# Kernel optimization log

Measured on AMD Instinct MI355X. Metric: run time of the kernel, lower is better.

The kernel has to match this reference:

```python
import jax, jax.numpy as jnp
import numpy as np

CHANNELS = [64, 128, 256, 512, 512]
RES = [256, 128, 64, 32, 16]
N = 8          # batch
NQ = 128       # n_quad
NCW = 128      # nc_w (output descriptor size)
GRAD_BOOST = 10.0


def _norm(x):
    # Norm module: per-sample, per-row normalization over last dim; torch std is unbiased (ddof=1)
    m = jnp.mean(x, axis=-1, keepdims=True)
    s = jnp.std(x, axis=-1, ddof=1, keepdims=True)
    return (x - m) / (s + 1e-8)


def _quad(x, w):
    # Quad_module: (M^T @ softmax(grad_boost*w, axis=0))**2, summed over spatial dim
    n, c, h, wd = x.shape
    M = x.reshape(n, c, h * wd)                      # (N, C, HW)
    sm = jax.nn.softmax(w * GRAD_BOOST, axis=0)      # (C, NQ)
    proj = jnp.einsum('nch,co->nho', M, sm)          # (N, HW, NQ)
    return jnp.sum(proj ** 2, axis=1)                # (N, NQ)


def setup_inputs() -> dict:
    key = jax.random.key(0)
    ks = jax.random.split(key, 20)
    inp = {}
    for i, (c, r) in enumerate(zip(CHANNELS, RES)):
        inp[f"x{i}"] = jax.random.normal(ks[i], (N, c, r, r), dtype=jnp.float32)
        # torch init: 5/grad_boost * rand(n_in, n_out) = 0.5 * U[0,1)
        inp[f"w1_{i}"] = 0.5 * jax.random.uniform(ks[5 + i], (c, NQ), dtype=jnp.float32)
    d_in = len(CHANNELS) * NQ
    inp["fc1_w"] = jax.random.normal(ks[10], (d_in, 512), dtype=jnp.float32) * 0.04
    inp["fc1_b"] = jnp.zeros((512,), dtype=jnp.float32)
    inp["fc2_w"] = jax.random.normal(ks[11], (512, 512), dtype=jnp.float32) * 0.04
    inp["fc2_b"] = jnp.zeros((512,), dtype=jnp.float32)
    inp["fc3_w"] = jax.random.normal(ks[12], (512, NCW), dtype=jnp.float32) * 0.04
    inp["fc3_b"] = jnp.zeros((NCW,), dtype=jnp.float32)
    return inp


def reference(x0, x1, x2, x3, x4, w1_0, w1_1, w1_2, w1_3, w1_4,
              fc1_w, fc1_b, fc2_w, fc2_b, fc3_w, fc3_b):
    xs = [x0, x1, x2, x3, x4]
    ws = [w1_0, w1_1, w1_2, w1_3, w1_4]
    feats = [_norm(_quad(x, w)) for x, w in zip(xs, ws)]  # each (N, NQ)
    h = jnp.concatenate(feats, axis=1)                    # (N, 5*NQ)
    h = jax.nn.leaky_relu(_norm(h @ fc1_w + fc1_b), 0.01)
    h = jax.nn.leaky_relu(_norm(h @ fc2_w + fc2_b), 0.01)
    return h @ fc3_w + fc3_b                              # (N, NCW)
```

## Files before the change

### kernel.cpp

```cpp
#include <hip/hip_runtime.h>
#include <hip/hip_bf16.h>
#include <stdint.h>

#define NQ 128
#define NLVL 5

typedef float  floatx4 __attribute__((ext_vector_type(4)));
typedef short  short8  __attribute__((ext_vector_type(8)));

__device__ __forceinline__ uint16_t f2bf(float f) {
    uint32_t u = __builtin_bit_cast(uint32_t, f);
    uint32_t r = u + 0x7FFFu + ((u >> 16) & 1u);
    return (uint16_t)(r >> 16);
}

struct SmParams {
    const float* w[NLVL];
    uint16_t*    smT[NLVL];
    int          C[NLVL];
};

__global__ __launch_bounds__(64) void softmax_kernel(SmParams p) {
    int b   = blockIdx.x;
    int lvl = b >> 7;
    int o   = b & 127;
    int C   = p.C[lvl];
    const float* w = p.w[lvl];
    int lane = threadIdx.x;
    float ev[8];
    int nIter = C >> 6;
    float mx = -1e30f;
    for (int it = 0; it < nIter; ++it) {
        float z = 10.0f * w[(size_t)(it * 64 + lane) * NQ + o];
        ev[it] = z;
        mx = fmaxf(mx, z);
    }
    #pragma unroll
    for (int s = 32; s; s >>= 1) mx = fmaxf(mx, __shfl_xor(mx, s));
    float sum = 0.f;
    for (int it = 0; it < nIter; ++it) { ev[it] = expf(ev[it] - mx); sum += ev[it]; }
    #pragma unroll
    for (int s = 32; s; s >>= 1) sum += __shfl_xor(sum, s);
    float inv = 1.0f / sum;
    uint16_t* dst = p.smT[lvl] + (size_t)o * C;
    for (int it = 0; it < nIter; ++it) dst[it * 64 + lane] = f2bf(ev[it] * inv);
}

struct QuadParams {
    const float*    x[NLVL];
    const uint16_t* smT[NLVL];
    float*          quad;
    int             C[NLVL];
    int             HW[NLVL];
    int             blk_base[NLVL];
};

__global__ __launch_bounds__(256) void quad_kernel(QuadParams p) {
    __shared__ __align__(16) short At[64 * 40];
    __shared__ __align__(16) short Bt[128 * 40];

    int bid = blockIdx.x;
    int lvl = 0;
    #pragma unroll
    for (int l = 1; l < NLVL; ++l) if (bid >= p.blk_base[l]) lvl = l;
    int rel = bid - p.blk_base[lvl];
    int n   = rel & 7;
    int ht  = rel >> 3;
    int C   = p.C[lvl];
    int HW  = p.HW[lvl];
    int h0  = ht * 64;

    const float*    xb  = p.x[lvl] + (size_t)n * C * HW + h0;
    const uint16_t* smT = p.smT[lvl];

    int t    = threadIdx.x;
    int wave = t >> 6;
    int lane = t & 63;
    int m    = lane & 15;
    int kg   = lane >> 4;

    floatx4 acc[4][2];
    floatx4 zero = {0.f, 0.f, 0.f, 0.f};
    #pragma unroll
    for (int i = 0; i < 4; ++i)
        #pragma unroll
        for (int j = 0; j < 2; ++j) acc[i][j] = zero;

    int c_l = (t & 15) * 2;
    int h_l = (t >> 4) * 4;

    for (int c0 = 0; c0 < C; c0 += 32) {
        const float* s1 = xb + (size_t)(c0 + c_l) * HW + h_l;
        float4 a4 = *(const float4*)s1;
        float4 b4 = *(const float4*)(s1 + HW);
        #pragma unroll
        for (int j = 0; j < 4; ++j) {
            uint32_t pk = (uint32_t)f2bf(((const float*)&a4)[j]) |
                          ((uint32_t)f2bf(((const float*)&b4)[j]) << 16);
            *(uint32_t*)&At[(h_l + j) * 40 + c_l] = pk;
        }
        #pragma unroll
        for (int it = 0; it < 2; ++it) {
            int idx  = it * 256 + t;
            int o    = idx >> 2;
            int part = idx & 3;
            uint4 v = *(const uint4*)(smT + (size_t)o * C + c0 + part * 8);
            *(uint4*)&Bt[o * 40 + part * 8] = v;
        }
        __syncthreads();

        short8 af[4];
        #pragma unroll
        for (int mt = 0; mt < 4; ++mt)
            af[mt] = *(const short8*)&At[(mt * 16 + m) * 40 + kg * 8];
        short8 bfr[2];
        #pragma unroll
        for (int ot = 0; ot < 2; ++ot)
            bfr[ot] = *(const short8*)&Bt[((wave * 2 + ot) * 16 + m) * 40 + kg * 8];
        #pragma unroll
        for (int mt = 0; mt < 4; ++mt)
            #pragma unroll
            for (int ot = 0; ot < 2; ++ot)
                acc[mt][ot] = __builtin_amdgcn_mfma_f32_16x16x32_bf16(
                    af[mt], bfr[ot], acc[mt][ot], 0, 0, 0);
        __syncthreads();
    }

    float* qbase = p.quad + (size_t)(lvl * 8 + n) * 128 * 16;
    #pragma unroll
    for (int ot = 0; ot < 2; ++ot) {
        float part = 0.f;
        #pragma unroll
        for (int mt = 0; mt < 4; ++mt)
            #pragma unroll
            for (int r = 0; r < 4; ++r) {
                float v = acc[mt][ot][r];
                part = fmaf(v, v, part);
            }
        part += __shfl_xor(part, 16);
        part += __shfl_xor(part, 32);
        if (lane < 16) {
            int o = (wave * 2 + ot) * 16 + lane;
            atomicAdd(qbase + (size_t)o * 16, part);
        }
    }
}

__device__ __forceinline__ float block_sum512(float v, float* red8, int t) {
    #pragma unroll
    for (int s = 32; s; s >>= 1) v += __shfl_xor(v, s);
    __syncthreads();
    if ((t & 63) == 0) red8[t >> 6] = v;
    __syncthreads();
    float tot = 0.f;
    #pragma unroll
    for (int i = 0; i < 8; ++i) tot += red8[i];
    return tot;
}

__global__ __launch_bounds__(512) void head_kernel(
    const float* __restrict__ quad,
    const float* __restrict__ fc1_w, const float* __restrict__ fc1_b,
    const float* __restrict__ fc2_w, const float* __restrict__ fc2_b,
    const float* __restrict__ fc3_w, const float* __restrict__ fc3_b,
    float* __restrict__ out) {
    __shared__ float feat[640];
    __shared__ float hbuf[512];
    __shared__ float red8[8];
    __shared__ float stats[10];
    int n = blockIdx.x;
    int t = threadIdx.x;

    for (int idx = t; idx < 640; idx += 512) {
        int lvl = idx >> 7, o = idx & 127;
        feat[idx] = quad[((size_t)(lvl * 8 + n) * 128 + o) * 16];
    }
    __syncthreads();
    if (t < 5) {
        float s = 0.f;
        for (int i = 0; i < 128; ++i) s += feat[t * 128 + i];
        float mean = s * (1.f / 128.f);
        float v = 0.f;
        for (int i = 0; i < 128; ++i) { float d = feat[t * 128 + i] - mean; v += d * d; }
        stats[t]     = mean;
        stats[5 + t] = sqrtf(v * (1.f / 127.f)) + 1e-8f;
    }
    __syncthreads();
    for (int idx = t; idx < 640; idx += 512) {
        int lvl = idx >> 7;
        feat[idx] = (feat[idx] - stats[lvl]) / stats[5 + lvl];
    }
    __syncthreads();

    float acc = fc1_b[t];
    #pragma unroll 8
    for (int i = 0; i < 640; ++i) acc = fmaf(feat[i], fc1_w[(size_t)i * 512 + t], acc);
    float mean = block_sum512(acc, red8, t) * (1.f / 512.f);
    float d    = acc - mean;
    float var  = block_sum512(d * d, red8, t) * (1.f / 511.f);
    float nv   = d / (sqrtf(var) + 1e-8f);
    __syncthreads();
    hbuf[t] = nv > 0.f ? nv : 0.01f * nv;
    __syncthreads();

    float acc2 = fc2_b[t];
    #pragma unroll 8
    for (int i = 0; i < 512; ++i) acc2 = fmaf(hbuf[i], fc2_w[(size_t)i * 512 + t], acc2);
    mean = block_sum512(acc2, red8, t) * (1.f / 512.f);
    d    = acc2 - mean;
    var  = block_sum512(d * d, red8, t) * (1.f / 511.f);
    nv   = d / (sqrtf(var) + 1e-8f);
    __syncthreads();
    hbuf[t] = nv > 0.f ? nv : 0.01f * nv;
    __syncthreads();

    if (t < 128) {
        float acc3 = fc3_b[t];
        #pragma unroll 8
        for (int i = 0; i < 512; ++i) acc3 = fmaf(hbuf[i], fc3_w[(size_t)i * 128 + t], acc3);
        out[(size_t)n * 128 + t] = acc3;
    }
}

extern "C" void kernel_launch(void* const* d_in, const int* in_sizes, int n_in,
                              void* d_out, int out_size, void* d_ws, size_t ws_size,
                              hipStream_t stream) {
    static const int Cs[NLVL]  = {64, 128, 256, 512, 512};
    static const int RESs[NLVL] = {256, 128, 64, 32, 16};

    const float* x[NLVL];
    const float* w[NLVL];
    for (int i = 0; i < NLVL; ++i) {
        x[i] = (const float*)d_in[2 * i];
        w[i] = (const float*)d_in[2 * i + 1];
    }
    const float* fc1_w = (const float*)d_in[10];
    const float* fc1_b = (const float*)d_in[11];
    const float* fc2_w = (const float*)d_in[12];
    const float* fc2_b = (const float*)d_in[13];
    const float* fc3_w = (const float*)d_in[14];
    const float* fc3_b = (const float*)d_in[15];

    uint16_t* smT_base = (uint16_t*)d_ws;
    int smOff[NLVL];
    int off = 0;
    for (int i = 0; i < NLVL; ++i) { smOff[i] = off; off += Cs[i] * NQ; }
    size_t smBytes = (size_t)off * sizeof(uint16_t);
    float* quad = (float*)((char*)d_ws + smBytes);
    size_t quadBytes = (size_t)NLVL * 8 * NQ * 16 * sizeof(float);

    SmParams sp;
    for (int i = 0; i < NLVL; ++i) {
        sp.w[i]   = w[i];
        sp.smT[i] = smT_base + smOff[i];
        sp.C[i]   = Cs[i];
    }
    softmax_kernel<<<NLVL * NQ, 64, 0, stream>>>(sp);

    hipMemsetAsync(quad, 0, quadBytes, stream);

    QuadParams qp;
    int base = 0;
    for (int i = 0; i < NLVL; ++i) {
        qp.x[i]   = x[i];
        qp.smT[i] = smT_base + smOff[i];
        qp.C[i]   = Cs[i];
        qp.HW[i]  = RESs[i] * RESs[i];
        qp.blk_base[i] = base;
        base += (RESs[i] * RESs[i] / 64) * 8;
    }
    qp.quad = quad;
    quad_kernel<<<base, 256, 0, stream>>>(qp);

    head_kernel<<<8, 512, 0, stream>>>(quad, fc1_w, fc1_b, fc2_w, fc2_b,
                                       fc3_w, fc3_b, (float*)d_out);
}
```

Baseline: 446.0 us.

## Compute quad features for large levels via Gram matrix instead of projection

```diff
diff --git a/kernel.cpp b/kernel.cpp
--- a/kernel.cpp
+++ b/kernel.cpp
@@ -12,6 +12,12 @@
     uint32_t u = __builtin_bit_cast(uint32_t, f);
     uint32_t r = u + 0x7FFFu + ((u >> 16) & 1u);
     return (uint16_t)(r >> 16);
+}
+__device__ __forceinline__ uint32_t pack2(float a, float b) {
+    return (uint32_t)f2bf(a) | ((uint32_t)f2bf(b) << 16);
+}
+__device__ __forceinline__ float bf2f(uint16_t u) {
+    return __builtin_bit_cast(float, (uint32_t)u << 16);
 }
 
 struct SmParams {
@@ -46,6 +52,187 @@
     for (int it = 0; it < nIter; ++it) dst[it * 64 + lane] = f2bf(ev[it] * inv);
 }
 
+struct GramParams { const float* x0; const float* x1; float* g0; float* g1; };
+
+template<int C, int HW, int NS>
+__device__ __forceinline__ void gram_body(const float* __restrict__ xb,
+                                          float* __restrict__ gb,
+                                          int h0, short* lds) {
+    constexpr int RF   = C / 64;
+    constexpr int CF   = C / 16;
+    constexpr int PASS = C / 16;
+    constexpr int STR  = 72;
+
+    int t    = threadIdx.x;
+    int wv   = t >> 6, lane = t & 63, m = lane & 15, kg = lane >> 4;
+    int rrow = t >> 4;
+    int rcol = (t & 15) * 4;
+    const float* src = xb + (size_t)rrow * HW + rcol + h0;
+
+    floatx4 acc[RF][CF];
+    floatx4 zero = {0.f, 0.f, 0.f, 0.f};
+    #pragma unroll
+    for (int rf = 0; rf < RF; ++rf)
+        #pragma unroll
+        for (int cf = 0; cf < CF; ++cf) acc[rf][cf] = zero;
+
+    float4 pf[PASS];
+    #pragma unroll
+    for (int p = 0; p < PASS; ++p) pf[p] = *(const float4*)(src + (size_t)p * 16 * HW);
+    #pragma unroll
+    for (int p = 0; p < PASS; ++p) {
+        uint2 pk = { pack2(pf[p].x, pf[p].y), pack2(pf[p].z, pf[p].w) };
+        *(uint2*)&lds[(p * 16 + rrow) * STR + rcol] = pk;
+    }
+
+    int cur = 0;
+    for (int s = 0; s < NS; ++s) {
+        if (s + 1 < NS) {
+            const float* s2 = src + (s + 1) * 64;
+            #pragma unroll
+            for (int p = 0; p < PASS; ++p) pf[p] = *(const float4*)(s2 + (size_t)p * 16 * HW);
+        }
+        __syncthreads();
+        const short* bc = lds + cur * (C * STR);
+        #pragma unroll
+        for (int ksl = 0; ksl < 2; ++ksl) {
+            short8 fr[CF], af[RF];
+            #pragma unroll
+            for (int f = 0; f < CF; ++f)
+                fr[f] = *(const short8*)&bc[(f * 16 + m) * STR + ksl * 32 + kg * 8];
+            #pragma unroll
+            for (int rf = 0; rf < RF; ++rf)
+                af[rf] = *(const short8*)&bc[((wv * RF + rf) * 16 + m) * STR + ksl * 32 + kg * 8];
+            #pragma unroll
+            for (int rf = 0; rf < RF; ++rf)
+                #pragma unroll
+                for (int cf = 0; cf < CF; ++cf)
+                    acc[rf][cf] = __builtin_amdgcn_mfma_f32_16x16x32_bf16(
+                        af[rf], fr[cf], acc[rf][cf], 0, 0, 0);
+        }
+        if (s + 1 < NS) {
+            short* bn = lds + (cur ^ 1) * (C * STR);
+            #pragma unroll
+            for (int p = 0; p < PASS; ++p) {
+                uint2 pk = { pack2(pf[p].x, pf[p].y), pack2(pf[p].z, pf[p].w) };
+                *(uint2*)&bn[(p * 16 + rrow) * STR + rcol] = pk;
+            }
+        }
+        cur ^= 1;
+    }
+
+    #pragma unroll
+    for (int rf = 0; rf < RF; ++rf) {
+        int row0 = (wv * RF + rf) * 16 + kg * 4;
+        #pragma unroll
+        for (int cf = 0; cf < CF; ++cf) {
+            int col = cf * 16 + m;
+            #pragma unroll
+            for (int r = 0; r < 4; ++r)
+                atomicAdd(&gb[(size_t)(row0 + r) * C + col], acc[rf][cf][r]);
+        }
+    }
+}
+
+__global__ __launch_bounds__(256) void gram_kernel(GramParams p) {
+    __shared__ __align__(16) short lds[2 * 128 * 72];
+    int b = blockIdx.x;
+    if (b < 512) {
+        int n = b >> 6, ch = b & 63;
+        gram_body<64, 65536, 16>(p.x0 + (size_t)n * 64 * 65536,
+                                 p.g0 + (size_t)n * 64 * 64, ch * 1024, lds);
+    } else {
+        int b2 = b - 512;
+        int n = b2 >> 5, ch = b2 & 31;
+        gram_body<128, 16384, 8>(p.x1 + (size_t)n * 128 * 16384,
+                                 p.g1 + (size_t)n * 128 * 128, ch * 512, lds);
+    }
+}
+
+struct SgsParams {
+    const float* g0; const float* g1;
+    const uint16_t* smT0; const uint16_t* smT1;
+    float* quad;
+};
+
+template<int C>
+__device__ __forceinline__ void sgs_body(const float* __restrict__ g,
+                                         const uint16_t* __restrict__ smT,
+                                         float* __restrict__ qdst, short* Gt) {
+    constexpr int RF  = C / 64;
+    constexpr int KSL = C / 32;
+    constexpr int STR = C + 8;
+    int t = threadIdx.x;
+    short* Ghi = Gt;
+    short* Glo = Gt + C * STR;
+    for (int i = t; i < C * C / 4; i += 256) {
+        int row = i / (C / 4);
+        int c4  = (i % (C / 4)) * 4;
+        float4 v = *(const float4*)(g + (size_t)row * C + c4);
+        uint16_t h0 = f2bf(v.x), h1 = f2bf(v.y), h2 = f2bf(v.z), h3 = f2bf(v.w);
+        uint2 ph = { (uint32_t)h0 | ((uint32_t)h1 << 16),
+                     (uint32_t)h2 | ((uint32_t)h3 << 16) };
+        uint2 pl = { pack2(v.x - bf2f(h0), v.y - bf2f(h1)),
+                     pack2(v.z - bf2f(h2), v.w - bf2f(h3)) };
+        *(uint2*)&Ghi[row * STR + c4] = ph;
+        *(uint2*)&Glo[row * STR + c4] = pl;
+    }
+    __syncthreads();
+    int wv = t >> 6, lane = t & 63, m = lane & 15, kg = lane >> 4;
+    floatx4 acc[RF][8];
+    floatx4 zero = {0.f, 0.f, 0.f, 0.f};
+    #pragma unroll
+    for (int rf = 0; rf < RF; ++rf)
+        #pragma unroll
+        for (int ot = 0; ot < 8; ++ot) acc[rf][ot] = zero;
+
+    #pragma unroll
+    for (int ksl = 0; ksl < KSL; ++ksl) {
+        short8 bf[8];
+        #pragma unroll
+        for (int ot = 0; ot < 8; ++ot)
+            bf[ot] = *(const short8*)(smT + (size_t)(ot * 16 + m) * C + ksl * 32 + kg * 8);
+        #pragma unroll
+        for (int rf = 0; rf < RF; ++rf) {
+            int roff = ((wv * RF + rf) * 16 + m) * STR + ksl * 32 + kg * 8;
+            short8 ah = *(const short8*)&Ghi[roff];
+            short8 al = *(const short8*)&Glo[roff];
+            #pragma unroll
+            for (int ot = 0; ot < 8; ++ot) {
+                acc[rf][ot] = __builtin_amdgcn_mfma_f32_16x16x32_bf16(ah, bf[ot], acc[rf][ot], 0, 0, 0);
+                acc[rf][ot] = __builtin_amdgcn_mfma_f32_16x16x32_bf16(al, bf[ot], acc[rf][ot], 0, 0, 0);
+            }
+        }
+    }
+    #pragma unroll
+    for (int ot = 0; ot < 8; ++ot) {
+        float part = 0.f;
+        #pragma unroll
+        for (int rf = 0; rf < RF; ++rf) {
+            int c0 = (wv * RF + rf) * 16 + kg * 4;
+            #pragma unroll
+            for (int r = 0; r < 4; ++r) {
+                float sv = bf2f(smT[(size_t)(ot * 16 + m) * C + c0 + r]);
+                part = fmaf(sv, acc[rf][ot][r], part);
+            }
+        }
+        part += __shfl_xor(part, 16);
+        part += __shfl_xor(part, 32);
+        if (lane < 16) atomicAdd(qdst + (size_t)(ot * 16 + lane) * 16, part);
+    }
+}
+
+__global__ __launch_bounds__(256) void sgs_kernel(SgsParams p) {
+    __shared__ __align__(16) short Gt[2 * 128 * 136];
+    int b = blockIdx.x, lvl = b >> 3, n = b & 7;
+    if (lvl == 0)
+        sgs_body<64>(p.g0 + (size_t)n * 64 * 64, p.smT0,
+                     p.quad + (size_t)n * 128 * 16, Gt);
+    else
+        sgs_body<128>(p.g1 + (size_t)n * 128 * 128, p.smT1,
+                      p.quad + (size_t)(8 + n) * 128 * 16, Gt);
+}
+
 struct QuadParams {
     const float*    x[NLVL];
     const uint16_t* smT[NLVL];
@@ -62,7 +249,7 @@
     int bid = blockIdx.x;
     int lvl = 0;
     #pragma unroll
-    for (int l = 1; l < NLVL; ++l) if (bid >= p.blk_base[l]) lvl = l;
+    for (int l = 1; l < 3; ++l) if (bid >= p.blk_base[l]) lvl = l;
     int rel = bid - p.blk_base[lvl];
     int n   = rel & 7;
     int ht  = rel >> 3;
@@ -126,7 +313,7 @@
         __syncthreads();
     }
 
-    float* qbase = p.quad + (size_t)(lvl * 8 + n) * 128 * 16;
+    float* qbase = p.quad + (size_t)((lvl + 2) * 8 + n) * 128 * 16;
     #pragma unroll
     for (int ot = 0; ot < 2; ++ot) {
         float part = 0.f;
@@ -225,7 +412,7 @@
 extern "C" void kernel_launch(void* const* d_in, const int* in_sizes, int n_in,
                               void* d_out, int out_size, void* d_ws, size_t ws_size,
                               hipStream_t stream) {
-    static const int Cs[NLVL]  = {64, 128, 256, 512, 512};
+    static const int Cs[NLVL]   = {64, 128, 256, 512, 512};
     static const int RESs[NLVL] = {256, 128, 64, 32, 16};
 
     const float* x[NLVL];
@@ -247,7 +434,10 @@
     for (int i = 0; i < NLVL; ++i) { smOff[i] = off; off += Cs[i] * NQ; }
     size_t smBytes = (size_t)off * sizeof(uint16_t);
     float* quad = (float*)((char*)d_ws + smBytes);
-    size_t quadBytes = (size_t)NLVL * 8 * NQ * 16 * sizeof(float);
+    size_t quadFloats = (size_t)NLVL * 8 * NQ * 16;
+    float* g0 = quad + quadFloats;
+    float* g1 = g0 + (size_t)8 * 64 * 64;
+    size_t zeroBytes = (quadFloats + (size_t)8 * 64 * 64 + (size_t)8 * 128 * 128) * sizeof(float);
 
     SmParams sp;
     for (int i = 0; i < NLVL; ++i) {
@@ -257,21 +447,37 @@
     }
     softmax_kernel<<<NLVL * NQ, 64, 0, stream>>>(sp);
 
-    hipMemsetAsync(quad, 0, quadBytes, stream);
+    hipMemsetAsync(quad, 0, zeroBytes, stream);
+
+    GramParams gp;
+    gp.x0 = x[0]; gp.x1 = x[1]; gp.g0 = g0; gp.g1 = g1;
+    gram_kernel<<<768, 256, 0, stream>>>(gp);
 
     QuadParams qp;
     int base = 0;
-    for (int i = 0; i < NLVL; ++i) {
-        qp.x[i]   = x[i];
-        qp.smT[i] = smT_base + smOff[i];
-        qp.C[i]   = Cs[i];
-        qp.HW[i]  = RESs[i] * RESs[i];
+    for (int i = 0; i < 3; ++i) {
+        int lvl = i + 2;
+        qp.x[i]   = x[lvl];
+        qp.smT[i] = smT_base + smOff[lvl];
+        qp.C[i]   = Cs[lvl];
+        qp.HW[i]  = RESs[lvl] * RESs[lvl];
         qp.blk_base[i] = base;
-        base += (RESs[i] * RESs[i] / 64) * 8;
+        base += (RESs[lvl] * RESs[lvl] / 64) * 8;
+    }
+    for (int i = 3; i < NLVL; ++i) {
+        qp.x[i] = nullptr; qp.smT[i] = nullptr;
+        qp.C[i] = 0; qp.HW[i] = 0; qp.blk_base[i] = 0x7fffffff;
     }
     qp.quad = quad;
     quad_kernel<<<base, 256, 0, stream>>>(qp);
 
+    SgsParams ssp;
+    ssp.g0 = g0; ssp.g1 = g1;
+    ssp.smT0 = smT_base + smOff[0];
+    ssp.smT1 = smT_base + smOff[1];
+    ssp.quad = quad;
+    sgs_kernel<<<16, 256, 0, stream>>>(ssp);
+
     head_kernel<<<8, 512, 0, stream>>>(quad, fc1_w, fc1_b, fc2_w, fc2_b,
                                        fc3_w, fc3_b, (float*)d_out);
 }
```

After: 461.9 us. 3.6% more time.
